# Optimization experiments

Hardware: AMD Instinct MI355X
Metric: run time of the kernel (lower is better)

The kernel has to match this reference:

```python
import jax, jax.numpy as jnp
import numpy as np

B, S = 2, 2048
HQ, HKV, D = 32, 8, 128
SCALING = 0.08838834764831845  # 1/sqrt(128)
E4M3_MAX = 448.0
FP4_MAX = 6.0
# e2m1 representable magnitudes and decision midpoints
FP4_GRID = jnp.array([0.0, 0.5, 1.0, 1.5, 2.0, 3.0, 4.0, 6.0], dtype=jnp.float32)
FP4_MID = (FP4_GRID[:-1] + FP4_GRID[1:]) / 2.0


def quant_dequant_e4m3(x):
    """Simulate torch .to(float8_e4m3fn): clamp to +-448, round mantissa to 3 bits."""
    ax = jnp.abs(x)
    xc = jnp.clip(x, -E4M3_MAX, E4M3_MAX)
    e = jnp.clip(jnp.floor(jnp.log2(jnp.maximum(ax, 1e-12))), -6.0, 8.0)
    q = jnp.round(xc * jnp.exp2(3.0 - e)) * jnp.exp2(e - 3.0)
    return jnp.where(ax == 0.0, 0.0, q)


def quant_dequant_fp4(x):
    """FP4 (e2m1) compress/decompress with per-(token,head) absmax scale over head_dim.
    x: [B, S, H, D] -> dequantized [B, S, H, D]."""
    scale = jnp.max(jnp.abs(x), axis=-1, keepdims=True) / FP4_MAX  # [B,S,H,1]
    scale = jnp.maximum(scale, 1e-12)
    xn = x / scale
    idx = jnp.searchsorted(FP4_MID, jnp.abs(xn))  # nearest e2m1 magnitude
    return jnp.sign(xn) * FP4_GRID[idx] * scale


def setup_inputs() -> dict:
    key = jax.random.key(0)
    kq, kk, kv = jax.random.split(key, 3)
    q = jax.random.normal(kq, (B, S, HQ * D), dtype=jnp.float32)
    k = jax.random.normal(kk, (B, S, HKV * D), dtype=jnp.float32)
    v = jax.random.normal(kv, (B, S, HKV * D), dtype=jnp.float32)
    return {"q": q, "k": k, "v": v}


def reference(q, k, v):
    # reshape to heads
    qh = q.reshape(B, S, HQ, D)
    kh = k.reshape(B, S, HKV, D)
    vh = v.reshape(B, S, HKV, D)
    # FP8 cast then FP4 compress/decompress of the KV cache
    kq8 = quant_dequant_e4m3(kh)
    vq8 = quant_dequant_e4m3(vh)
    kd = quant_dequant_fp4(kq8)
    vd = quant_dequant_fp4(vq8)
    # GQA: expand kv heads to query heads
    g = HQ // HKV
    kr = jnp.repeat(kd, g, axis=2)  # [B,S,HQ,D]
    vr = jnp.repeat(vd, g, axis=2)
    scores = jnp.einsum("bqhd,bkhd->bhqk", qh, kr) * SCALING  # [B,HQ,S,S]
    causal = jnp.tril(jnp.ones((S, S), dtype=bool))
    scores = jnp.where(causal[None, None], scores, jnp.float32(-1e30))
    probs = jax.nn.softmax(scores, axis=-1)
    out = jnp.einsum("bhqk,bkhd->bqhd", probs, vr)
    return out.reshape(B, S, HQ * D)
```

## Files before the change

### kernel.cpp

```cpp
#include <hip/hip_runtime.h>
#include <cstdint>
#include <cstddef>

#define B_    2
#define S_    2048
#define HQ_   32
#define HKV_  8
#define D_    128
#define QSCALE_ (0.08838834764831845f * 1.4426950408889634f)

#define NROW_ (B_*S_*HKV_)

typedef __bf16 bf16x8 __attribute__((ext_vector_type(8)));
typedef float  f32x4  __attribute__((ext_vector_type(4)));

__device__ __forceinline__ unsigned short f2bfu(float f) {
    __bf16 b = (__bf16)f;
    return __builtin_bit_cast(unsigned short, b);
}

__device__ __forceinline__ void gl_lds16(const unsigned short* g, unsigned short* l) {
    __builtin_amdgcn_global_load_lds(
        (const __attribute__((address_space(1))) void*)g,
        (__attribute__((address_space(3))) void*)l, 16, 0, 0);
}

__device__ __forceinline__ float qd_e4m3(float x) {
    float ax = fabsf(x);
    float xc = fminf(fmaxf(x, -448.f), 448.f);
    float axc = fmaxf(ax, 1e-12f);
    int e = (int)((__builtin_bit_cast(unsigned int, axc) >> 23) & 255u) - 127;
    e = min(max(e, -6), 8);
    float s1 = __builtin_bit_cast(float, (unsigned int)(130 - e) << 23);
    float s2 = __builtin_bit_cast(float, (unsigned int)(124 + e) << 23);
    float q = rintf(xc * s1) * s2;
    return ax == 0.f ? 0.f : q;
}

__device__ __forceinline__ float qd_fp4(float x, float scale) {
    float xn = x / scale;
    float a = fabsf(xn);
    float g;
    if      (a <= 0.25f) g = 0.f;
    else if (a <= 0.75f) g = 0.5f;
    else if (a <= 1.25f) g = 1.f;
    else if (a <= 1.75f) g = 1.5f;
    else if (a <= 2.5f)  g = 2.f;
    else if (a <= 3.5f)  g = 3.f;
    else if (a <= 5.f)   g = 4.f;
    else                 g = 6.f;
    return copysignf(g * scale, xn);
}

__global__ __launch_bounds__(256) void quant_kv(const float* __restrict__ k,
                                                const float* __restrict__ v,
                                                unsigned short* __restrict__ kd,
                                                unsigned short* __restrict__ vd) {
    int gw = (blockIdx.x * 256 + threadIdx.x) >> 6;
    int lane = threadIdx.x & 63;
    int row = gw;
    const float* src;
    unsigned short* dst;
    if (row < NROW_) { src = k; dst = kd; }
    else             { row -= NROW_; src = v; dst = vd; }
    int b   = row / (S_ * HKV_);
    int rem = row - b * (S_ * HKV_);
    int s   = rem >> 3;
    int h   = rem & 7;
    float2 x = *(const float2*)(src + (size_t)row * D_ + 2 * lane);
    float q0 = qd_e4m3(x.x);
    float q1 = qd_e4m3(x.y);
    float amax = fmaxf(fabsf(q0), fabsf(q1));
#pragma unroll
    for (int m = 1; m < 64; m <<= 1) amax = fmaxf(amax, __shfl_xor(amax, m, 64));
    float scale = fmaxf(amax / 6.0f, 1e-12f);
    float y0 = qd_fp4(q0, scale);
    float y1 = qd_fp4(q1, scale);
    size_t outOff = ((size_t)(b * HKV_ + h) * S_ + s) * D_ + 2 * lane;
    unsigned int pack = (unsigned int)f2bfu(y0) | ((unsigned int)f2bfu(y1) << 16);
    *(unsigned int*)(dst + outOff) = pack;
}

__global__ __launch_bounds__(256) void transpose_v(const unsigned short* __restrict__ vd,
                                                   unsigned short* __restrict__ vdT) {
    __shared__ alignas(16) unsigned short t[64][136];
    int bh = blockIdx.x >> 5;
    int st = blockIdx.x & 31;
    int s0 = st * 64;
    int tid = threadIdx.x;
    {
        int row = tid >> 2;
        const unsigned short* sp = vd + ((size_t)bh * S_ + s0 + row) * D_;
#pragma unroll
        for (int i = 0; i < 4; ++i) {
            int c = (tid & 3) + 4 * i;
            *(uint4*)&t[row][c * 8] = *(const uint4*)(sp + c * 8);
        }
    }
    __syncthreads();
    {
        int d = tid >> 1;
        unsigned short* dp = vdT + ((size_t)bh * D_ + d) * S_ + s0;
#pragma unroll
        for (int i = 0; i < 4; ++i) {
            int c = (tid & 1) + 2 * i;
            int so = c * 8;
            unsigned short tmp[8];
#pragma unroll
            for (int e = 0; e < 8; ++e) tmp[e] = t[so + e][d];
            *(uint4*)(dp + so) = *(uint4*)tmp;
        }
    }
}

__global__ __launch_bounds__(256) void attn(const float* __restrict__ q,
                                            const unsigned short* __restrict__ kd,
                                            const unsigned short* __restrict__ vdT,
                                            float* __restrict__ out) {
    int bh = blockIdx.x;
    int yp = blockIdx.y;
    int b  = bh >> 5;
    int hq = bh & 31;
    int hkv = hq >> 2;
    int tid  = threadIdx.x;
    int lane = tid & 63;
    int wave = tid >> 6;
    int m16  = lane & 15;
    int g    = lane >> 4;
    int m8   = m16 & 7;

    __shared__ alignas(16) unsigned short ks[64 * 128];
    __shared__ alignas(16) unsigned short vs[128 * 64];
    __shared__ alignas(16) unsigned short ps[4 * 16 * 64];

    const unsigned short* kbase = kd  + (size_t)(b * HKV_ + hkv) * S_ * D_;
    const unsigned short* vbase = vdT + (size_t)(b * HKV_ + hkv) * D_ * S_;

    bf16x8 vones;
#pragma unroll
    for (int j = 0; j < 8; ++j) vones[j] = (__bf16)1.0f;

    for (int phase = 0; phase < 2; ++phase) {
        int qt = phase ? yp : (31 - yp);
        int q0 = qt * 64;
        int qrowBase = q0 + wave * 16;

        bf16x8 qf[4];
        const float* qp = q + (((size_t)b * S_ + (qrowBase + m16)) * HQ_ + hq) * D_;
#pragma unroll
        for (int c = 0; c < 4; ++c) {
            const float* p0 = qp + c * 32 + g * 8;
            bf16x8 f;
#pragma unroll
            for (int j = 0; j < 8; ++j) f[j] = (__bf16)(p0[j] * QSCALE_);
            qf[c] = f;
        }

        f32x4 o[8];
#pragma unroll
        for (int i = 0; i < 8; ++i) o[i] = (f32x4){0.f, 0.f, 0.f, 0.f};
        f32x4 o9 = (f32x4){0.f, 0.f, 0.f, 0.f};

        for (int kt = 0; kt <= qt; ++kt) {
            int k0 = kt * 64;
            __syncthreads();
#pragma unroll
            for (int i = 0; i < 4; ++i) {
                int row = wave * 16 + i * 4 + (lane >> 4);
                int c = (lane & 15) ^ (row & 15);
                gl_lds16(kbase + (size_t)(k0 + row) * D_ + c * 8,
                         &ks[wave * 2048 + i * 512]);
            }
#pragma unroll
            for (int i = 0; i < 4; ++i) {
                int d = wave * 32 + i * 8 + (lane >> 3);
                int c = (lane & 7) ^ (d & 7);
                gl_lds16(vbase + (size_t)d * S_ + k0 + c * 8,
                         &vs[wave * 2048 + i * 512]);
            }
            __syncthreads();

            bool diag = (kt == qt);
            int kcmax = diag ? ((wave >> 1) + 1) : 2;

            f32x4 sacc[4];
#pragma unroll
            for (int n = 0; n < 4; ++n) sacc[n] = (f32x4){0.f, 0.f, 0.f, 0.f};
#pragma unroll
            for (int n = 0; n < 4; ++n) {
                if (!diag || n <= wave) {
#pragma unroll
                    for (int c = 0; c < 4; ++c) {
                        bf16x8 ak = *(const bf16x8*)&ks[(n * 16 + m16) * 128 +
                                                        (((c * 4 + g) ^ m16) * 8)];
                        sacc[n] = __builtin_amdgcn_mfma_f32_16x16x32_bf16(ak, qf[c], sacc[n], 0, 0, 0);
                    }
                }
            }

            int qloc = wave * 16 + m16;
            float pv[4][4];
#pragma unroll
            for (int n = 0; n < 4; ++n) {
                if (!diag || n <= wave) {
#pragma unroll
                    for (int r = 0; r < 4; ++r) {
                        float p = exp2f(sacc[n][r]);
                        if (diag) {
                            int key = n * 16 + g * 4 + r;
                            p = (key <= qloc) ? p : 0.f;
                        }
                        pv[n][r] = p;
                    }
                }
            }

#pragma unroll
            for (int n = 0; n < 4; ++n) {
                if (n < 2 * kcmax) {
                    unsigned int lo = 0, hi = 0;
                    if (!diag || n <= wave) {
                        lo = (unsigned int)f2bfu(pv[n][0]) | ((unsigned int)f2bfu(pv[n][1]) << 16);
                        hi = (unsigned int)f2bfu(pv[n][2]) | ((unsigned int)f2bfu(pv[n][3]) << 16);
                    }
                    int chunk = (n * 2 + (g >> 1)) ^ m8;
                    uint2 val; val.x = lo; val.y = hi;
                    *(uint2*)&ps[wave * 1024 + m16 * 64 + chunk * 8 + (g & 1) * 4] = val;
                }
            }
            asm volatile("s_waitcnt lgkmcnt(0)" ::: "memory");

#pragma unroll
            for (int kc = 0; kc < 2; ++kc) {
                if (kc < kcmax) {
                    bf16x8 pa = *(const bf16x8*)&ps[wave * 1024 + m16 * 64 +
                                                    (((kc * 4 + g) ^ m8) * 8)];
                    o9 = __builtin_amdgcn_mfma_f32_16x16x32_bf16(pa, vones, o9, 0, 0, 0);
#pragma unroll
                    for (int ds = 0; ds < 8; ++ds) {
                        bf16x8 vb = *(const bf16x8*)&vs[(ds * 16 + m16) * 64 +
                                                        (((kc * 4 + g) ^ m8) * 8)];
                        o[ds] = __builtin_amdgcn_mfma_f32_16x16x32_bf16(pa, vb, o[ds], 0, 0, 0);
                    }
                }
            }
        }

#pragma unroll
        for (int r = 0; r < 4; ++r) {
            float inv = 1.f / o9[r];
            float* op = out + (((size_t)b * S_ + (qrowBase + g * 4 + r)) * HQ_ + hq) * D_;
#pragma unroll
            for (int ds = 0; ds < 8; ++ds)
                op[ds * 16 + m16] = o[ds][r] * inv;
        }
    }
}

extern "C" void kernel_launch(void* const* d_in, const int* in_sizes, int n_in,
                              void* d_out, int out_size, void* d_ws, size_t ws_size,
                              hipStream_t stream) {
    const float* q = (const float*)d_in[0];
    const float* k = (const float*)d_in[1];
    const float* v = (const float*)d_in[2];
    float* out = (float*)d_out;

    unsigned short* kd  = (unsigned short*)d_ws;
    unsigned short* vd  = kd + (size_t)NROW_ * D_;
    unsigned short* vdT = vd + (size_t)NROW_ * D_;

    quant_kv<<<16384, 256, 0, stream>>>(k, v, kd, vd);
    transpose_v<<<512, 256, 0, stream>>>(vd, vdT);
    attn<<<dim3(64, 16), 256, 0, stream>>>(q, kd, vdT, out);
}
```

Baseline: 259.2 us.

## Double query tile per block to 128 rows, two 16-row slabs per wave

Each block now handles a 128-row query tile, with each wave holding two 16-row query slabs, so every K/V tile loaded into LDS feeds twice as many MFMAs. Causal masking moves from a per-wave diagonal flag to per-slab bounds computed from the query/key offset. The grid is halved to 64x8, which cuts global K/V traffic and barrier count per unit of work. In exchange it doubles accumulator registers per wave, which may lower occupancy, and the fewer blocks may hurt load balance.

Result: slower. 266.2 us (+2.7%).

```diff
diff --git a/kernel.cpp b/kernel.cpp
--- a/kernel.cpp
+++ b/kernel.cpp
@@ -131,7 +131,7 @@
 
     __shared__ alignas(16) unsigned short ks[64 * 128];
     __shared__ alignas(16) unsigned short vs[128 * 64];
-    __shared__ alignas(16) unsigned short ps[4 * 16 * 64];
+    __shared__ alignas(16) unsigned short ps[8 * 16 * 64];
 
     const unsigned short* kbase = kd  + (size_t)(b * HKV_ + hkv) * S_ * D_;
     const unsigned short* vbase = vdT + (size_t)(b * HKV_ + hkv) * D_ * S_;
@@ -141,27 +141,35 @@
     for (int j = 0; j < 8; ++j) vones[j] = (__bf16)1.0f;
 
     for (int phase = 0; phase < 2; ++phase) {
-        int qt = phase ? yp : (31 - yp);
-        int q0 = qt * 64;
-        int qrowBase = q0 + wave * 16;
-
-        bf16x8 qf[4];
-        const float* qp = q + (((size_t)b * S_ + (qrowBase + m16)) * HQ_ + hq) * D_;
-#pragma unroll
-        for (int c = 0; c < 4; ++c) {
-            const float* p0 = qp + c * 32 + g * 8;
-            bf16x8 f;
-#pragma unroll
-            for (int j = 0; j < 8; ++j) f[j] = (__bf16)(p0[j] * QSCALE_);
-            qf[c] = f;
+        int qt = phase ? yp : (15 - yp);
+        int q0 = qt * 128;
+        int qs0 = q0 + wave * 32;
+        int ktot = 2 * qt + 2;
+
+        bf16x8 qf[2][4];
+#pragma unroll
+        for (int s = 0; s < 2; ++s) {
+            const float* qp = q + (((size_t)b * S_ + (qs0 + s * 16 + m16)) * HQ_ + hq) * D_;
+#pragma unroll
+            for (int c = 0; c < 4; ++c) {
+                const float* p0 = qp + c * 32 + g * 8;
+                bf16x8 f;
+#pragma unroll
+                for (int j = 0; j < 8; ++j) f[j] = (__bf16)(p0[j] * QSCALE_);
+                qf[s][c] = f;
+            }
         }
 
-        f32x4 o[8];
-#pragma unroll
-        for (int i = 0; i < 8; ++i) o[i] = (f32x4){0.f, 0.f, 0.f, 0.f};
-        f32x4 o9 = (f32x4){0.f, 0.f, 0.f, 0.f};
-
-        for (int kt = 0; kt <= qt; ++kt) {
+        f32x4 o[2][8];
+#pragma unroll
+        for (int s = 0; s < 2; ++s)
+#pragma unroll
+            for (int i = 0; i < 8; ++i) o[s][i] = (f32x4){0.f, 0.f, 0.f, 0.f};
+        f32x4 o9[2];
+        o9[0] = (f32x4){0.f, 0.f, 0.f, 0.f};
+        o9[1] = (f32x4){0.f, 0.f, 0.f, 0.f};
+
+        for (int kt = 0; kt < ktot; ++kt) {
             int k0 = kt * 64;
             __syncthreads();
 #pragma unroll
@@ -180,80 +188,104 @@
             }
             __syncthreads();
 
-            bool diag = (kt == qt);
-            int kcmax = diag ? ((wave >> 1) + 1) : 2;
-
-            f32x4 sacc[4];
-#pragma unroll
-            for (int n = 0; n < 4; ++n) sacc[n] = (f32x4){0.f, 0.f, 0.f, 0.f};
+            int dq0 = qs0 - k0;
+            int e0 = dq0 + 15;
+            int e1 = dq0 + 31;
+            int nmax0 = min(4, max(0, (e0 >> 4) + 1));
+            int nmax1 = min(4, max(0, (e1 >> 4) + 1));
+            int kc0   = min(2, max(0, (e0 >> 5) + 1));
+            int kc1   = min(2, max(0, (e1 >> 5) + 1));
+
+            f32x4 sa[2][4];
+#pragma unroll
+            for (int s = 0; s < 2; ++s)
+#pragma unroll
+                for (int n = 0; n < 4; ++n) sa[s][n] = (f32x4){0.f, 0.f, 0.f, 0.f};
 #pragma unroll
             for (int n = 0; n < 4; ++n) {
-                if (!diag || n <= wave) {
+                if (n < nmax1) {
 #pragma unroll
                     for (int c = 0; c < 4; ++c) {
                         bf16x8 ak = *(const bf16x8*)&ks[(n * 16 + m16) * 128 +
                                                         (((c * 4 + g) ^ m16) * 8)];
-                        sacc[n] = __builtin_amdgcn_mfma_f32_16x16x32_bf16(ak, qf[c], sacc[n], 0, 0, 0);
+                        if (n < nmax0)
+                            sa[0][n] = __builtin_amdgcn_mfma_f32_16x16x32_bf16(ak, qf[0][c], sa[0][n], 0, 0, 0);
+                        sa[1][n] = __builtin_amdgcn_mfma_f32_16x16x32_bf16(ak, qf[1][c], sa[1][n], 0, 0, 0);
                     }
                 }
             }
 
-            int qloc = wave * 16 + m16;
-            float pv[4][4];
-#pragma unroll
-            for (int n = 0; n < 4; ++n) {
-                if (!diag || n <= wave) {
-#pragma unroll
-                    for (int r = 0; r < 4; ++r) {
-                        float p = exp2f(sacc[n][r]);
-                        if (diag) {
-                            int key = n * 16 + g * 4 + r;
-                            p = (key <= qloc) ? p : 0.f;
+#pragma unroll
+            for (int s = 0; s < 2; ++s) {
+                int nmx = s ? nmax1 : nmax0;
+                int kcm = s ? kc1 : kc0;
+                int dqs = dq0 + s * 16;
+#pragma unroll
+                for (int n = 0; n < 4; ++n) {
+                    if (n < 2 * kcm) {
+                        uint2 val; val.x = 0u; val.y = 0u;
+                        if (n < nmx) {
+                            bool needMask = (n * 16 + 15 > dqs);
+                            float pr[4];
+#pragma unroll
+                            for (int r = 0; r < 4; ++r) {
+                                float p = exp2f(sa[s][n][r]);
+                                if (needMask)
+                                    p = (n * 16 + g * 4 + r <= dqs + m16) ? p : 0.f;
+                                pr[r] = p;
+                            }
+                            val.x = (unsigned int)f2bfu(pr[0]) | ((unsigned int)f2bfu(pr[1]) << 16);
+                            val.y = (unsigned int)f2bfu(pr[2]) | ((unsigned int)f2bfu(pr[3]) << 16);
                         }
-                        pv[n][r] = p;
+                        int chunk = (n * 2 + (g >> 1)) ^ m8;
+                        *(uint2*)&ps[(wave * 2 + s) * 1024 + m16 * 64 + chunk * 8 + (g & 1) * 4] = val;
                     }
                 }
             }
-
-#pragma unroll
-            for (int n = 0; n < 4; ++n) {
-                if (n < 2 * kcmax) {
-                    unsigned int lo = 0, hi = 0;
-                    if (!diag || n <= wave) {
-                        lo = (unsigned int)f2bfu(pv[n][0]) | ((unsigned int)f2bfu(pv[n][1]) << 16);
-                        hi = (unsigned int)f2bfu(pv[n][2]) | ((unsigned int)f2bfu(pv[n][3]) << 16);
-                    }
-                    int chunk = (n * 2 + (g >> 1)) ^ m8;
-                    uint2 val; val.x = lo; val.y = hi;
-                    *(uint2*)&ps[wave * 1024 + m16 * 64 + chunk * 8 + (g & 1) * 4] = val;
-                }
-            }
             asm volatile("s_waitcnt lgkmcnt(0)" ::: "memory");
 
+            bf16x8 pa[2][2];
+#pragma unroll
+            for (int s = 0; s < 2; ++s) {
+                int kcm = s ? kc1 : kc0;
+#pragma unroll
+                for (int kc = 0; kc < 2; ++kc)
+                    if (kc < kcm)
+                        pa[s][kc] = *(const bf16x8*)&ps[(wave * 2 + s) * 1024 + m16 * 64 +
+                                                        (((kc * 4 + g) ^ m8) * 8)];
+            }
 #pragma unroll
             for (int kc = 0; kc < 2; ++kc) {
-                if (kc < kcmax) {
-                    bf16x8 pa = *(const bf16x8*)&ps[wave * 1024 + m16 * 64 +
-                                                    (((kc * 4 + g) ^ m8) * 8)];
-                    o9 = __builtin_amdgcn_mfma_f32_16x16x32_bf16(pa, vones, o9, 0, 0, 0);
-#pragma unroll
-                    for (int ds = 0; ds < 8; ++ds) {
+                if (kc < kc0)
+                    o9[0] = __builtin_amdgcn_mfma_f32_16x16x32_bf16(pa[0][kc], vones, o9[0], 0, 0, 0);
+                if (kc < kc1)
+                    o9[1] = __builtin_amdgcn_mfma_f32_16x16x32_bf16(pa[1][kc], vones, o9[1], 0, 0, 0);
+            }
+#pragma unroll
+            for (int ds = 0; ds < 8; ++ds) {
+#pragma unroll
+                for (int kc = 0; kc < 2; ++kc) {
+                    if (kc < kc1) {
                         bf16x8 vb = *(const bf16x8*)&vs[(ds * 16 + m16) * 64 +
                                                         (((kc * 4 + g) ^ m8) * 8)];
-                        o[ds] = __builtin_amdgcn_mfma_f32_16x16x32_bf16(pa, vb, o[ds], 0, 0, 0);
+                        if (kc < kc0)
+                            o[0][ds] = __builtin_amdgcn_mfma_f32_16x16x32_bf16(pa[0][kc], vb, o[0][ds], 0, 0, 0);
+                        o[1][ds] = __builtin_amdgcn_mfma_f32_16x16x32_bf16(pa[1][kc], vb, o[1][ds], 0, 0, 0);
                     }
                 }
             }
         }
 
 #pragma unroll
-        for (int r = 0; r < 4; ++r) {
-            float inv = 1.f / o9[r];
-            float* op = out + (((size_t)b * S_ + (qrowBase + g * 4 + r)) * HQ_ + hq) * D_;
-#pragma unroll
-            for (int ds = 0; ds < 8; ++ds)
-                op[ds * 16 + m16] = o[ds][r] * inv;
-        }
+        for (int s = 0; s < 2; ++s)
+#pragma unroll
+            for (int r = 0; r < 4; ++r) {
+                float inv = 1.f / o9[s][r];
+                float* op = out + (((size_t)b * S_ + (qs0 + s * 16 + g * 4 + r)) * HQ_ + hq) * D_;
+#pragma unroll
+                for (int ds = 0; ds < 8; ++ds)
+                    op[ds * 16 + m16] = o[s][ds][r] * inv;
+            }
     }
 }
 
@@ -271,5 +303,5 @@
 
     quant_kv<<<16384, 256, 0, stream>>>(k, v, kd, vd);
     transpose_v<<<512, 256, 0, stream>>>(vd, vdT);
-    attn<<<dim3(64, 16), 256, 0, stream>>>(q, kd, vdT, out);
-}
+    attn<<<dim3(64, 8), 256, 0, stream>>>(q, kd, vdT, out);
+}
```
